# Performance work log

Hardware: AMD Instinct MI355X
Metric: run time of the kernel (lower is better)

Reference implementation:

```python
import jax, jax.numpy as jnp
import numpy as np

B, S = 8, 128
D_SENS, D_ACT, D_STR, D_ENC, DIM = 512, 32, 128, 128, 128
D_JOINT = D_STR + D_ENC  # 256


def _l2norm(x):
    return x / jnp.clip(jnp.linalg.norm(x, axis=-1, keepdims=True), 1e-12)


def _mlp(x, layers):
    # layers: list of (W, b); ReLU between layers, none on output
    n = len(layers)
    for i, (W, b) in enumerate(layers):
        x = x @ W + b
        if i < n - 1:
            x = jax.nn.relu(x)
    return x


def _meta_mlp(x, p):
    x = jax.nn.relu(x @ p['W1'] + p['b1'])
    x = jax.nn.relu(x @ p['W2'] + p['b2'])
    return x @ p['W3'] + p['b3']


def setup_inputs() -> dict:
    key = jax.random.key(0)
    it = iter(jax.random.split(key, 40))
    w = lambda shape, s=0.02: jax.random.normal(next(it), shape, jnp.float32) * s
    H = D_ACT * 4  # to_transitions hidden dim (default mlp_hidden_dim)
    return dict(
        sensory=jax.random.normal(next(it), (B, S, D_SENS), jnp.float32),
        actions=jax.random.normal(next(it), (B, S, D_ACT), jnp.float32),
        init_hidden=w((1, D_STR), 0.01),
        tW1=w((D_ACT, H)), tb1=w((H,)),
        tW2=w((H, H)), tb2=w((H,)),
        tW3=w((H, D_STR * D_STR)), tb3=w((D_STR * D_STR,)),
        enc_w=w((D_SENS, D_ENC)), enc_b=w((D_ENC,)),
        dec_w=w((D_ENC, D_SENS)), dec_b=w((D_SENS,)),
        q_w=w((D_JOINT, DIM)), k_w=w((D_JOINT, DIM)), v_w=w((D_JOINT, DIM)),
        mW1=w((DIM, 2 * DIM)), mb1=w((2 * DIM,)),
        mW2=w((2 * DIM, 2 * DIM)), mb2=w((2 * DIM,)),
        mW3=w((2 * DIM, DIM)), mb3=w((DIM,)),
        oW1=w((DIM, 2 * DIM)), ob1=w((2 * DIM,)),
        oW2=w((2 * DIM, 2 * DIM)), ob2=w((2 * DIM,)),
        oW3=w((2 * DIM, D_JOINT)), ob3=w((D_JOINT,)),
        sW1=w((2 * D_STR + 1, 2 * D_STR)), sb1=w((2 * D_STR,)),
        sW2=w((2 * D_STR, 2 * D_STR)), sb2=w((2 * D_STR,)),
        sW3=w((2 * D_STR, D_STR)), sb3=w((D_STR,)),
        integration_ratio=jnp.asarray(0.1, jnp.float32),
    )


def reference(sensory, actions, init_hidden, tW1, tb1, tW2, tb2, tW3, tb3,
              enc_w, enc_b, dec_w, dec_b, q_w, k_w, v_w,
              mW1, mb1, mW2, mb2, mW3, mb3,
              oW1, ob1, oW2, ob2, oW3, ob3,
              sW1, sb1, sW2, sb2, sW3, sb3, integration_ratio):
    mse = lambda a, b: jnp.mean((a - b) ** 2)

    # --- PathIntegration: actions -> transitions -> scripted RNN scan ---
    trans = _mlp(actions, [(tW1, tb1), (tW2, tb2), (tW3, tb3)])  # (B,S,ds*ds)
    trans = trans.reshape(B, S, D_STR, D_STR)
    h0 = jnp.broadcast_to(_l2norm(init_hidden), (B, D_STR))

    def step(h, T):  # h (B,ds), T (B,ds,ds)
        h = _l2norm(jax.nn.relu(jnp.einsum('bi,bij->bj', h, T)))
        return h, h

    _, hs = jax.lax.scan(step, h0, jnp.swapaxes(trans, 0, 1))
    structural = jnp.swapaxes(hs, 0, 1)  # (B,S,ds)

    # --- sensory encoder (Linear) ---
    encoded = sensory @ enc_w + enc_b  # (B,S,D_ENC)

    meta_params = {'W1': mW1, 'b1': mb1, 'W2': mW2, 'b2': mb2, 'W3': mW3, 'b3': mb3}

    def retrieve(s, e):
        joint = jnp.concatenate((s, e), axis=-1)
        q = joint @ q_w
        r = _meta_mlp(q, meta_params)
        out = _mlp(r, [(oW1, ob1), (oW2, ob2), (oW3, ob3)])
        return out[..., :D_STR], out[..., D_STR:]

    # generative branch
    dec_gen_s, dec_enc = retrieve(structural, jnp.zeros_like(encoded))
    generative_pred_loss = mse(sensory, dec_enc @ dec_w + dec_b)

    # relational branch (source calls retrieve(zeros, encoded) twice)
    dec_s1, _ = retrieve(jnp.zeros_like(structural), encoded)
    dec_s2, _ = retrieve(jnp.zeros_like(structural), encoded)
    relational_loss = mse(dec_s1, structural) + mse(dec_s2, structural)

    # consistency / inference correction
    corr_s, corr_e = retrieve(dec_gen_s, encoded)
    sse = jnp.sum((corr_e - encoded) ** 2, axis=-1, keepdims=True)  # (B,S,1)
    pred_var = _mlp(jnp.concatenate((corr_s, dec_gen_s, sse), axis=-1),
                    [(sW1, sb1), (sW2, sb2), (sW3, sb3)])
    inf_s = dec_gen_s + (corr_s - dec_gen_s) * integration_ratio * pred_var
    consistency_loss = mse(dec_gen_s, inf_s)

    final_s, inf_e = retrieve(inf_s, jnp.zeros_like(encoded))
    inference_pred_loss = mse(sensory, inf_e @ dec_w + dec_b)

    # per-sample fast-weight memory gradients (nested vmap(grad))
    store = jnp.concatenate((final_s, encoded), axis=-1)
    keys = store @ k_w
    values = store @ v_w

    def meta_loss(p, k, v):
        return jnp.mean((_meta_mlp(k, p) - v) ** 2)

    per_grad = jax.vmap(jax.vmap(jax.grad(meta_loss), in_axes=(None, 0, 0)),
                        in_axes=(None, 0, 0))
    g = per_grad(meta_params, keys, values)  # each leaf (B,S,*param_shape)

    total = (generative_pred_loss + relational_loss
             + consistency_loss + inference_pred_loss)  # all loss weights 1.0
    return (total, g['W1'], g['b1'], g['W2'], g['b2'], g['W3'], g['b3'])
```

## Files before the change

### kernel.cpp

```cpp
#include <hip/hip_runtime.h>
#include <hip/hip_bf16.h>

constexpr size_t OFF_W1 = 1;
constexpr size_t OFF_B1 = OFF_W1 + (size_t)1024*32768;
constexpr size_t OFF_W2 = OFF_B1 + (size_t)1024*256;
constexpr size_t OFF_B2 = OFF_W2 + (size_t)1024*65536;
constexpr size_t OFF_W3 = OFF_B2 + (size_t)1024*256;
constexpr size_t OFF_B3 = OFF_W3 + (size_t)1024*32768;

__global__ __launch_bounds__(256) void gemm_kernel(
    const float* __restrict__ A, int lda,
    const float* __restrict__ W, int ldw,
    const float* __restrict__ bias,
    float* __restrict__ C, int ldc,
    int N, int K, int do_relu)
{
    __shared__ float As[16][65];
    __shared__ float Ws[16][65];
    const int tid = threadIdx.x;
    const int tx = tid & 15, ty = tid >> 4;
    const int m0 = blockIdx.x * 64, n0 = blockIdx.y * 64;
    float acc[4][4] = {};
    for (int k0 = 0; k0 < K; k0 += 16) {
        for (int l = tid; l < 1024; l += 256) {
            int mm = l >> 4, kk = l & 15;
            int gk = k0 + kk;
            As[kk][mm] = (gk < K) ? A[(size_t)(m0+mm)*lda + gk] : 0.f;
        }
        for (int l = tid; l < 1024; l += 256) {
            int kk = l >> 6, nn = l & 63;
            int gk = k0 + kk, gn = n0 + nn;
            Ws[kk][nn] = (gk < K && gn < N) ? W[(size_t)gk*ldw + gn] : 0.f;
        }
        __syncthreads();
        #pragma unroll
        for (int kk = 0; kk < 16; ++kk) {
            float a[4], b[4];
            #pragma unroll
            for (int i=0;i<4;i++) a[i] = As[kk][ty*4+i];
            #pragma unroll
            for (int j=0;j<4;j++) b[j] = Ws[kk][tx*4+j];
            #pragma unroll
            for (int i=0;i<4;i++)
                #pragma unroll
                for (int j=0;j<4;j++)
                    acc[i][j] = fmaf(a[i], b[j], acc[i][j]);
        }
        __syncthreads();
    }
    #pragma unroll
    for (int i=0;i<4;i++){
        int gm = m0 + ty*4 + i;
        #pragma unroll
        for (int j=0;j<4;j++){
            int gn = n0 + tx*4 + j;
            if (gn < N) {
                float v = acc[i][j] + (bias ? bias[gn] : 0.f);
                if (do_relu) v = fmaxf(v, 0.f);
                C[(size_t)gm*ldc + gn] = v;
            }
        }
    }
}

__global__ __launch_bounds__(512) void scan_kernel2(
    const float* __restrict__ trans,
    const float* __restrict__ init_hidden,
    float* __restrict__ structural)
{
    __shared__ float h[128];
    __shared__ float psum[16*128];
    const int b = blockIdx.x, tid = threadIdx.x;
    const int q = tid >> 5, g = tid & 31;
    const int jj = g * 4, i0 = q * 8;

    if (tid < 32) {
        float4 v = *(const float4*)&init_hidden[tid*4];
        float ss = v.x*v.x + v.y*v.y + v.z*v.z + v.w*v.w;
        ss += __shfl_xor(ss, 16); ss += __shfl_xor(ss, 8); ss += __shfl_xor(ss, 4);
        ss += __shfl_xor(ss, 2);  ss += __shfl_xor(ss, 1);
        float inv = 1.f / fmaxf(sqrtf(ss), 1e-12f);
        v.x *= inv; v.y *= inv; v.z *= inv; v.w *= inv;
        *(float4*)&h[tid*4] = v;
    }
    __syncthreads();

    float4 cur[8], nxt[8];
    {
        const float* T0 = trans + ((size_t)(b*128) << 14);
        #pragma unroll
        for (int i = 0; i < 8; ++i)
            cur[i] = *(const float4*)&T0[(size_t)(i0+i)*128 + jj];
    }

    for (int t = 0; t < 128; ++t) {
        const int tn = (t < 127) ? t + 1 : 127;
        const float* Tn = trans + ((size_t)(b*128 + tn) << 14);
        #pragma unroll
        for (int i = 0; i < 8; ++i)
            nxt[i] = *(const float4*)&Tn[(size_t)(i0+i)*128 + jj];

        float4 acc = make_float4(0.f,0.f,0.f,0.f);
        #pragma unroll
        for (int i = 0; i < 8; ++i) {
            float hv = h[i0+i];
            acc.x = fmaf(hv, cur[i].x, acc.x);
            acc.y = fmaf(hv, cur[i].y, acc.y);
            acc.z = fmaf(hv, cur[i].z, acc.z);
            acc.w = fmaf(hv, cur[i].w, acc.w);
        }
        *(float4*)&psum[q*128 + jj] = acc;
        __syncthreads();
        if (tid < 32) {
            float4 s = make_float4(0.f,0.f,0.f,0.f);
            #pragma unroll
            for (int qq = 0; qq < 16; ++qq) {
                float4 p = *(const float4*)&psum[qq*128 + tid*4];
                s.x += p.x; s.y += p.y; s.z += p.z; s.w += p.w;
            }
            s.x = fmaxf(s.x, 0.f); s.y = fmaxf(s.y, 0.f);
            s.z = fmaxf(s.z, 0.f); s.w = fmaxf(s.w, 0.f);
            float ss = s.x*s.x + s.y*s.y + s.z*s.z + s.w*s.w;
            ss += __shfl_xor(ss, 16); ss += __shfl_xor(ss, 8); ss += __shfl_xor(ss, 4);
            ss += __shfl_xor(ss, 2);  ss += __shfl_xor(ss, 1);
            float inv = 1.f / fmaxf(sqrtf(ss), 1e-12f);
            s.x *= inv; s.y *= inv; s.z *= inv; s.w *= inv;
            *(float4*)&h[tid*4] = s;
            *(float4*)&structural[((size_t)(b*128 + t))*128 + tid*4] = s;
        }
        __syncthreads();
        #pragma unroll
        for (int i = 0; i < 8; ++i) cur[i] = nxt[i];
    }
}

__device__ __forceinline__ void stage_rows(float* buf, const float* src, int ld,
                                           int row0, int rows, int t)
{
    int r = t >> 5; if (rows == 4) r &= 3;
    const int k4 = (t & 31) * 4;
    float4 v = make_float4(0.f,0.f,0.f,0.f);
    if (src) v = *(const float4*)&src[(size_t)(row0 + r)*ld + k4];
    *(float4*)&buf[r*128 + k4] = v;
}

__device__ __forceinline__ void layer_n256_r8(
    const float* __restrict__ W, const float* __restrict__ bias, int K,
    const float* __restrict__ x, int xs, float* __restrict__ y, int relu, int t)
{
    const int c4 = (t & 63) * 4;
    const int r0 = (t >> 6) * 2;
    float4 a0 = bias ? *(const float4*)&bias[c4] : make_float4(0.f,0.f,0.f,0.f);
    float4 a1 = a0;
    const float* x0 = x + r0 * xs;
    const float* x1 = x0 + xs;
    for (int k = 0; k < K; ++k) {
        float4 w = *(const float4*)&W[(size_t)k*256 + c4];
        float xa = x0[k], xb = x1[k];
        a0.x = fmaf(w.x, xa, a0.x); a0.y = fmaf(w.y, xa, a0.y);
        a0.z = fmaf(w.z, xa, a0.z); a0.w = fmaf(w.w, xa, a0.w);
        a1.x = fmaf(w.x, xb, a1.x); a1.y = fmaf(w.y, xb, a1.y);
        a1.z = fmaf(w.z, xb, a1.z); a1.w = fmaf(w.w, xb, a1.w);
    }
    if (relu) {
        a0.x=fmaxf(a0.x,0.f); a0.y=fmaxf(a0.y,0.f); a0.z=fmaxf(a0.z,0.f); a0.w=fmaxf(a0.w,0.f);
        a1.x=fmaxf(a1.x,0.f); a1.y=fmaxf(a1.y,0.f); a1.z=fmaxf(a1.z,0.f); a1.w=fmaxf(a1.w,0.f);
    }
    *(float4*)&y[r0*256 + c4] = a0;
    *(float4*)&y[(r0+1)*256 + c4] = a1;
}

__device__ __forceinline__ void layer_n256_r4(
    const float* __restrict__ W, const float* __restrict__ bias, int K,
    const float* __restrict__ x, int xs, float* __restrict__ y, int relu,
    const float* __restrict__ mask, int t)
{
    const int c4 = (t & 63) * 4;
    const int r = t >> 6;
    float4 a = bias ? *(const float4*)&bias[c4] : make_float4(0.f,0.f,0.f,0.f);
    const float* xr = x + r * xs;
    for (int k = 0; k < K; ++k) {
        float4 w = *(const float4*)&W[(size_t)k*256 + c4];
        float xa = xr[k];
        a.x = fmaf(w.x, xa, a.x); a.y = fmaf(w.y, xa, a.y);
        a.z = fmaf(w.z, xa, a.z); a.w = fmaf(w.w, xa, a.w);
    }
    if (relu) {
        a.x=fmaxf(a.x,0.f); a.y=fmaxf(a.y,0.f); a.z=fmaxf(a.z,0.f); a.w=fmaxf(a.w,0.f);
    }
    if (mask) {
        float4 m = *(const float4*)&mask[r*256 + c4];
        a.x = (m.x > 0.f) ? a.x : 0.f; a.y = (m.y > 0.f) ? a.y : 0.f;
        a.z = (m.z > 0.f) ? a.z : 0.f; a.w = (m.w > 0.f) ? a.w : 0.f;
    }
    *(float4*)&y[r*256 + c4] = a;
}

__device__ __forceinline__ void layer_n128(
    const float* __restrict__ W, const float* __restrict__ bias, int K,
    const float* __restrict__ x, int xs, float* __restrict__ y, int ys, int relu,
    int rows, int t)
{
    const int c4 = (t & 31) * 4;
    int r = t >> 5; if (rows == 4) r &= 3;
    float4 a = bias ? *(const float4*)&bias[c4] : make_float4(0.f,0.f,0.f,0.f);
    const float* xr = x + r * xs;
    for (int k = 0; k < K; ++k) {
        float4 w = *(const float4*)&W[(size_t)k*128 + c4];
        float xa = xr[k];
        a.x = fmaf(w.x, xa, a.x); a.y = fmaf(w.y, xa, a.y);
        a.z = fmaf(w.z, xa, a.z); a.w = fmaf(w.w, xa, a.w);
    }
    if (relu) {
        a.x=fmaxf(a.x,0.f); a.y=fmaxf(a.y,0.f); a.z=fmaxf(a.z,0.f); a.w=fmaxf(a.w,0.f);
    }
    *(float4*)&y[r*ys + c4] = a;
}

__device__ __forceinline__ void layer_n128_dual(
    const float* __restrict__ W,
    const float* __restrict__ xA, const float* __restrict__ xB,
    float* __restrict__ y, int rows, int t)
{
    const int c4 = (t & 31) * 4;
    int r = t >> 5; if (rows == 4) r &= 3;
    float4 a = make_float4(0.f,0.f,0.f,0.f);
    const float* xa_ = xA + r * 128;
    const float* xb_ = xB + r * 128;
    for (int k = 0; k < 128; ++k) {
        float4 w = *(const float4*)&W[(size_t)k*128 + c4];
        float v = xa_[k];
        a.x = fmaf(w.x, v, a.x); a.y = fmaf(w.y, v, a.y);
        a.z = fmaf(w.z, v, a.z); a.w = fmaf(w.w, v, a.w);
    }
    for (int k = 0; k < 128; ++k) {
        float4 w = *(const float4*)&W[(size_t)(128+k)*128 + c4];
        float v = xb_[k];
        a.x = fmaf(w.x, v, a.x); a.y = fmaf(w.y, v, a.y);
        a.z = fmaf(w.z, v, a.z); a.w = fmaf(w.w, v, a.w);
    }
    *(float4*)&y[r*128 + c4] = a;
}

__global__ __launch_bounds__(256) void fused_retrieve_kernel(
    const float* __restrict__ A1, int ld1,
    const float* __restrict__ A2, int ld2,
    const float* __restrict__ qw,
    const float* __restrict__ mW1, const float* __restrict__ mb1,
    const float* __restrict__ mW2, const float* __restrict__ mb2,
    const float* __restrict__ mW3, const float* __restrict__ mb3,
    const float* __restrict__ oW1, const float* __restrict__ ob1,
    const float* __restrict__ oW2, const float* __restrict__ ob2,
    const float* __restrict__ oW3, const float* __restrict__ ob3,
    float* __restrict__ outB)
{
    __shared__ float bufA[8*128], bufB[8*128], ping[8*256], pong[8*256];
    const int t = threadIdx.x;
    const int row0 = blockIdx.x * 8;

    stage_rows(bufA, A1, ld1, row0, 8, t);
    stage_rows(bufB, A2, ld2, row0, 8, t);
    __syncthreads();
    layer_n128_dual(qw, bufA, bufB, ping, 8, t);
    __syncthreads();
    layer_n256_r8(mW1, mb1, 128, ping, 128, pong, 1, t);
    __syncthreads();
    layer_n256_r8(mW2, mb2, 256, pong, 256, ping, 1, t);
    __syncthreads();
    layer_n128(mW3, mb3, 256, ping, 256, pong, 128, 0, 8, t);
    __syncthreads();
    layer_n256_r8(oW1, ob1, 128, pong, 128, ping, 1, t);
    __syncthreads();
    layer_n256_r8(oW2, ob2, 256, ping, 256, pong, 1, t);
    __syncthreads();
    layer_n256_r8(oW3, ob3, 256, pong, 256, ping, 0, t);
    __syncthreads();
    #pragma unroll
    for (int e = t; e < 512; e += 256) {
        int r = e >> 6, c = (e & 63) * 4;
        *(float4*)&outB[(size_t)(row0+r)*256 + c] = *(const float4*)&ping[r*256 + c];
    }
}

__global__ __launch_bounds__(256) void fused_svar_kernel(
    const float* __restrict__ out3,
    const float* __restrict__ out1,
    const float* __restrict__ encoded,
    const float* __restrict__ sW1, const float* __restrict__ sb1,
    const float* __restrict__ sW2, const float* __restrict__ sb2,
    const float* __restrict__ sW3, const float* __restrict__ sb3,
    float* __restrict__ pvar)
{
    __shared__ float bufA[8*128], bufB[8*128], sse[8], ping[8*256], pong[8*256];
    const int t = threadIdx.x;
    const int row0 = blockIdx.x * 8;
    const int r = t >> 5, k4 = (t & 31) * 4;

    {
        float4 cs = *(const float4*)&out3[(size_t)(row0+r)*256 + k4];
        float4 ds = *(const float4*)&out1[(size_t)(row0+r)*256 + k4];
        *(float4*)&bufA[r*128 + k4] = cs;
        *(float4*)&bufB[r*128 + k4] = ds;
        float4 ce = *(const float4*)&out3[(size_t)(row0+r)*256 + 128 + k4];
        float4 en = *(const float4*)&encoded[(size_t)(row0+r)*128 + k4];
        float dx = ce.x-en.x, dy = ce.y-en.y, dz = ce.z-en.z, dw = ce.w-en.w;
        float ss = dx*dx + dy*dy + dz*dz + dw*dw;
        ss += __shfl_xor(ss, 16); ss += __shfl_xor(ss, 8); ss += __shfl_xor(ss, 4);
        ss += __shfl_xor(ss, 2);  ss += __shfl_xor(ss, 1);
        if ((t & 31) == 0) sse[r] = ss;
    }
    __syncthreads();
    {
        const int c4 = (t & 63) * 4;
        const int r0 = (t >> 6) * 2;
        float4 a0 = *(const float4*)&sb1[c4];
        float4 a1 = a0;
        for (int k = 0; k < 128; ++k) {
            float4 w = *(const float4*)&sW1[(size_t)k*256 + c4];
            float xa = bufA[r0*128 + k], xb = bufA[(r0+1)*128 + k];
            a0.x=fmaf(w.x,xa,a0.x); a0.y=fmaf(w.y,xa,a0.y); a0.z=fmaf(w.z,xa,a0.z); a0.w=fmaf(w.w,xa,a0.w);
            a1.x=fmaf(w.x,xb,a1.x); a1.y=fmaf(w.y,xb,a1.y); a1.z=fmaf(w.z,xb,a1.z); a1.w=fmaf(w.w,xb,a1.w);
        }
        for (int k = 0; k < 128; ++k) {
            float4 w = *(const float4*)&sW1[(size_t)(128+k)*256 + c4];
            float xa = bufB[r0*128 + k], xb = bufB[(r0+1)*128 + k];
            a0.x=fmaf(w.x,xa,a0.x); a0.y=fmaf(w.y,xa,a0.y); a0.z=fmaf(w.z,xa,a0.z); a0.w=fmaf(w.w,xa,a0.w);
            a1.x=fmaf(w.x,xb,a1.x); a1.y=fmaf(w.y,xb,a1.y); a1.z=fmaf(w.z,xb,a1.z); a1.w=fmaf(w.w,xb,a1.w);
        }
        {
            float4 w = *(const float4*)&sW1[(size_t)256*256 + c4];
            float xa = sse[r0], xb = sse[r0+1];
            a0.x=fmaf(w.x,xa,a0.x); a0.y=fmaf(w.y,xa,a0.y); a0.z=fmaf(w.z,xa,a0.z); a0.w=fmaf(w.w,xa,a0.w);
            a1.x=fmaf(w.x,xb,a1.x); a1.y=fmaf(w.y,xb,a1.y); a1.z=fmaf(w.z,xb,a1.z); a1.w=fmaf(w.w,xb,a1.w);
        }
        a0.x=fmaxf(a0.x,0.f); a0.y=fmaxf(a0.y,0.f); a0.z=fmaxf(a0.z,0.f); a0.w=fmaxf(a0.w,0.f);
        a1.x=fmaxf(a1.x,0.f); a1.y=fmaxf(a1.y,0.f); a1.z=fmaxf(a1.z,0.f); a1.w=fmaxf(a1.w,0.f);
        *(float4*)&ping[r0*256 + c4] = a0;
        *(float4*)&ping[(r0+1)*256 + c4] = a1;
    }
    __syncthreads();
    layer_n256_r8(sW2, sb2, 256, ping, 256, pong, 1, t);
    __syncthreads();
    layer_n128(sW3, sb3, 256, pong, 256, ping, 128, 0, 8, t);
    __syncthreads();
    {
        int rr = t >> 5, c = (t & 31) * 4;
        *(float4*)&pvar[(size_t)(row0+rr)*128 + c] = *(const float4*)&ping[rr*128 + c];
    }
}

__global__ __launch_bounds__(256) void fused_grad_kernel(
    const float* __restrict__ A1,
    const float* __restrict__ encoded,
    const float* __restrict__ k_w, const float* __restrict__ v_w,
    const float* __restrict__ mW1, const float* __restrict__ mb1,
    const float* __restrict__ mW2, const float* __restrict__ mb2,
    const float* __restrict__ mW3, const float* __restrict__ mb3,
    const float* __restrict__ T2,
    const float* __restrict__ T3,
    float* __restrict__ out)
{
    __shared__ float bufA[4*128], bufB[4*128], ks[4*128], vs[4*128];
    __shared__ float h1[4*256], h2[4*256], dob[4*128], dh2[4*256], dh1[4*256];
    const int t = threadIdx.x;
    const int row0 = blockIdx.x * 4;

    stage_rows(bufA, A1, 256, row0, 4, t);
    stage_rows(bufB, encoded, 128, row0, 4, t);
    __syncthreads();
    layer_n128_dual(k_w, bufA, bufB, ks, 4, t);
    layer_n128_dual(v_w, bufA, bufB, vs, 4, t);
    __syncthreads();
    layer_n256_r4(mW1, mb1, 128, ks, 128, h1, 1, nullptr, t);
    __syncthreads();
    layer_n256_r4(mW2, mb2, 256, h1, 256, h2, 1, nullptr, t);
    __syncthreads();
    layer_n128(mW3, mb3, 256, h2, 256, dob, 128, 0, 4, t);
    __syncthreads();
    for (int e = t; e < 512; e += 256)
        dob[e] = (dob[e] - vs[e]) * 0.015625f;
    __syncthreads();
    layer_n256_r4(T3, nullptr, 128, dob, 128, dh2, 0, h2, t);
    __syncthreads();
    layer_n256_r4(T2, nullptr, 256, dh2, 256, dh1, 0, h1, t);
    __syncthreads();

    #pragma unroll
    for (int r = 0; r < 4; ++r) {
        const size_t row = row0 + r;
        {
            const float dv = dh1[r*256 + t];
            float* p = out + OFF_W1 + row*32768;
            for (int i = 0; i < 128; ++i)
                p[(size_t)i*256 + t] = ks[r*128 + i] * dv;
            out[OFF_B1 + row*256 + t] = dv;
        }
        {
            const float d2 = dh2[r*256 + t];
            float* p = out + OFF_W2 + row*65536;
            for (int i = 0; i < 256; ++i)
                p[(size_t)i*256 + t] = h1[r*256 + i] * d2;
            out[OFF_B2 + row*256 + t] = d2;
        }
        {
            const int j = t & 127, ih = t >> 7;
            const float d3 = dob[r*128 + j];
            float* p = out + OFF_W3 + row*32768;
            for (int i = ih*128; i < ih*128 + 128; ++i)
                p[(size_t)i*128 + j] = h2[r*256 + i] * d3;
            if (t < 128) out[OFF_B3 + row*128 + t] = dob[r*128 + t];
        }
    }
}

__global__ __launch_bounds__(256) void mse_kernel(
    const float* __restrict__ A, int lda,
    const float* __restrict__ Bm, int ldb,
    int N, float scale, float* __restrict__ accum)
{
    const int m = blockIdx.x;
    float s = 0.f;
    for (int jj = threadIdx.x; jj < N; jj += 256) {
        float d = A[(size_t)m*lda + jj] - Bm[(size_t)m*ldb + jj];
        s = fmaf(d, d, s);
    }
    #pragma unroll
    for (int off = 32; off > 0; off >>= 1) s += __shfl_down(s, off, 64);
    __shared__ float w[4];
    if ((threadIdx.x & 63) == 0) w[threadIdx.x >> 6] = s;
    __syncthreads();
    if (threadIdx.x == 0) atomicAdd(accum, (w[0]+w[1]+w[2]+w[3]) * scale);
}

__global__ __launch_bounds__(128) void infs_kernel(
    const float* __restrict__ out1,
    const float* __restrict__ out3,
    const float* __restrict__ pvar,
    const float* __restrict__ ratio_p,
    float* __restrict__ inf_s,
    float scale, float* __restrict__ accum)
{
    const int m = blockIdx.x, t = threadIdx.x;
    float ratio = ratio_p[0];
    float dgs = out1[(size_t)m*256 + t];
    float cs  = out3[(size_t)m*256 + t];
    float pv  = pvar[(size_t)m*128 + t];
    float delta = (cs - dgs) * ratio * pv;
    inf_s[(size_t)m*128 + t] = dgs + delta;
    float ss = delta * delta;
    #pragma unroll
    for (int off = 32; off > 0; off >>= 1) ss += __shfl_down(ss, off, 64);
    __shared__ float w2[2];
    if ((t & 63) == 0) w2[t >> 6] = ss;
    __syncthreads();
    if (t == 0) atomicAdd(accum, (w2[0] + w2[1]) * scale);
}

__global__ void transpose_kernel(const float* __restrict__ src, float* __restrict__ dst, int R, int C)
{
    const int c = blockIdx.x, r = threadIdx.x;
    dst[(size_t)c*R + r] = src[(size_t)r*C + c];
}

__global__ void zero_kernel(float* acc) {
    if (threadIdx.x < 8) acc[threadIdx.x] = 0.f;
}

__global__ void total_kernel(const float* acc, float* out) {
    if (threadIdx.x == 0)
        out[0] = acc[0] + acc[1] + acc[2] + acc[3];
}

static inline void gemmF(const float* A, int lda, const float* W, int ldw, const float* bias,
                         float* C, int N, int K, int relu, hipStream_t s)
{
    dim3 g(16, (N + 63) / 64);
    gemm_kernel<<<g, 256, 0, s>>>(A, lda, W, ldw, bias, C, N, N, K, relu);
}

extern "C" void kernel_launch(void* const* d_in, const int* in_sizes, int n_in,
                              void* d_out, int out_size, void* d_ws, size_t ws_size,
                              hipStream_t stream)
{
    const float* sensory     = (const float*)d_in[0];
    const float* actions     = (const float*)d_in[1];
    const float* init_hidden = (const float*)d_in[2];
    const float* tW1 = (const float*)d_in[3];  const float* tb1 = (const float*)d_in[4];
    const float* tW2 = (const float*)d_in[5];  const float* tb2 = (const float*)d_in[6];
    const float* tW3 = (const float*)d_in[7];  const float* tb3 = (const float*)d_in[8];
    const float* enc_w = (const float*)d_in[9];  const float* enc_b = (const float*)d_in[10];
    const float* dec_w = (const float*)d_in[11]; const float* dec_b = (const float*)d_in[12];
    const float* q_w = (const float*)d_in[13];
    const float* k_w = (const float*)d_in[14];
    const float* v_w = (const float*)d_in[15];
    const float* mW1 = (const float*)d_in[16]; const float* mb1 = (const float*)d_in[17];
    const float* mW2 = (const float*)d_in[18]; const float* mb2 = (const float*)d_in[19];
    const float* mW3 = (const float*)d_in[20]; const float* mb3 = (const float*)d_in[21];
    const float* oW1 = (const float*)d_in[22]; const float* ob1 = (const float*)d_in[23];
    const float* oW2 = (const float*)d_in[24]; const float* ob2 = (const float*)d_in[25];
    const float* oW3 = (const float*)d_in[26]; const float* ob3 = (const float*)d_in[27];
    const float* sW1 = (const float*)d_in[28]; const float* sb1 = (const float*)d_in[29];
    const float* sW2 = (const float*)d_in[30]; const float* sb2 = (const float*)d_in[31];
    const float* sW3 = (const float*)d_in[32]; const float* sb3 = (const float*)d_in[33];
    const float* ratio = (const float*)d_in[34];
    float* out = (float*)d_out;

    float* Wsp = (float*)d_ws;
    size_t off = 0;
    float* acc  = Wsp + off; off += 16;
    float* a1   = Wsp + off; off += (size_t)1024*128;
    float* a2   = Wsp + off; off += (size_t)1024*128;
    float* trans= Wsp + off; off += (size_t)1024*16384;
    float* structural = Wsp + off; off += (size_t)1024*128;
    float* encoded    = Wsp + off; off += (size_t)1024*128;
    float* out1 = Wsp + off; off += (size_t)1024*256;
    float* out2 = Wsp + off; off += (size_t)1024*256;
    float* out3 = Wsp + off; off += (size_t)1024*256;
    float* out4 = Wsp + off; off += (size_t)1024*256;
    float* pvar = Wsp + off; off += (size_t)1024*128;
    float* infs = Wsp + off; off += (size_t)1024*128;
    float* deco = Wsp + off; off += (size_t)1024*512;
    float* T2   = Wsp + off; off += (size_t)256*256;
    float* T3   = Wsp + off; off += (size_t)128*256;

    zero_kernel<<<1, 64, 0, stream>>>(acc);
    transpose_kernel<<<256, 256, 0, stream>>>(mW2, T2, 256, 256);
    transpose_kernel<<<128, 256, 0, stream>>>(mW3, T3, 256, 128);

    gemmF(actions, 32, tW1, 128, tb1, a1, 128, 32, 1, stream);
    gemmF(a1, 128, tW2, 128, tb2, a2, 128, 128, 1, stream);
    gemmF(a2, 128, tW3, 16384, tb3, trans, 16384, 128, 0, stream);
    gemmF(sensory, 512, enc_w, 128, enc_b, encoded, 128, 512, 0, stream);
    scan_kernel2<<<8, 512, 0, stream>>>(trans, init_hidden, structural);

    fused_retrieve_kernel<<<128, 256, 0, stream>>>(structural, 128, nullptr, 0, q_w,
        mW1, mb1, mW2, mb2, mW3, mb3, oW1, ob1, oW2, ob2, oW3, ob3, out1);
    gemmF(out1 + 128, 256, dec_w, 512, dec_b, deco, 512, 128, 0, stream);
    mse_kernel<<<1024, 256, 0, stream>>>(deco, 512, sensory, 512, 512, 1.f/524288.f, acc + 0);

    fused_retrieve_kernel<<<128, 256, 0, stream>>>(nullptr, 0, encoded, 128, q_w,
        mW1, mb1, mW2, mb2, mW3, mb3, oW1, ob1, oW2, ob2, oW3, ob3, out2);
    mse_kernel<<<1024, 256, 0, stream>>>(out2, 256, structural, 128, 128, 2.f/131072.f, acc + 1);

    fused_retrieve_kernel<<<128, 256, 0, stream>>>(out1, 256, encoded, 128, q_w,
        mW1, mb1, mW2, mb2, mW3, mb3, oW1, ob1, oW2, ob2, oW3, ob3, out3);
    fused_svar_kernel<<<128, 256, 0, stream>>>(out3, out1, encoded,
        sW1, sb1, sW2, sb2, sW3, sb3, pvar);
    infs_kernel<<<1024, 128, 0, stream>>>(out1, out3, pvar, ratio, infs, 1.f/131072.f, acc + 2);

    fused_retrieve_kernel<<<128, 256, 0, stream>>>(infs, 128, nullptr, 0, q_w,
        mW1, mb1, mW2, mb2, mW3, mb3, oW1, ob1, oW2, ob2, oW3, ob3, out4);
    gemmF(out4 + 128, 256, dec_w, 512, dec_b, deco, 512, 128, 0, stream);
    mse_kernel<<<1024, 256, 0, stream>>>(deco, 512, sensory, 512, 512, 1.f/524288.f, acc + 3);

    fused_grad_kernel<<<256, 256, 0, stream>>>(out4, encoded, k_w, v_w,
        mW1, mb1, mW2, mb2, mW3, mb3, T2, T3, out);

    total_kernel<<<1, 64, 0, stream>>>(acc, out);
}
```

Measured before the change: 1.533 ms.

## Transpose transition weights, fuse decoder GEMM with MSE, batch retrieve passes, vectorize grad stores

```diff
diff --git a/kernel.cpp b/kernel.cpp
--- a/kernel.cpp
+++ b/kernel.cpp
@@ -63,16 +63,135 @@
     }
 }
 
-__global__ __launch_bounds__(512) void scan_kernel2(
-    const float* __restrict__ trans,
+__global__ __launch_bounds__(256) void prep_kernel(
+    const float* __restrict__ tW3,
+    const float* __restrict__ mW2, const float* __restrict__ mW3,
+    float* __restrict__ tW3T,
+    float* __restrict__ T2, float* __restrict__ T3,
+    float* __restrict__ acc)
+{
+    __shared__ float tile[64*129];
+    const int t = threadIdx.x;
+    const int bid = blockIdx.x;
+    if (bid < 256) {
+        const int k = bid >> 1, i0 = (bid & 1) * 64;
+        const size_t base = (size_t)k << 14;
+        for (int l = t; l < 8192; l += 256) {
+            int ii = l >> 7, jj = l & 127;
+            tile[ii*129 + jj] = tW3[base + (size_t)(i0+ii)*128 + jj];
+        }
+        __syncthreads();
+        for (int l = t; l < 8192; l += 256) {
+            int jj = l >> 6, ii = l & 63;
+            tW3T[base + (size_t)jj*128 + i0 + ii] = tile[ii*129 + jj];
+        }
+    } else if (bid < 512) {
+        const int c = bid - 256;
+        T2[(size_t)c*256 + t] = mW2[(size_t)t*256 + c];
+    } else if (bid < 640) {
+        const int c = bid - 512;
+        T3[(size_t)c*256 + t] = mW3[(size_t)t*128 + c];
+    } else {
+        if (t < 16) acc[t] = 0.f;
+    }
+}
+
+__device__ __forceinline__ void gemm_k128_compute(
+    const float* __restrict__ A, int lda, const float* __restrict__ W,
+    const float* __restrict__ bias, int bias_mode, int N, int m0, int n0, int t,
+    float* __restrict__ As, float4* __restrict__ acc)
+{
+    for (int l = t; l < 4096; l += 256) {
+        int r = l >> 7, k = l & 127;
+        As[k*36 + r] = A[(size_t)(m0 + r)*lda + k];
+    }
+    __syncthreads();
+    const int c4 = (t & 63) * 4;
+    const int r0 = (t >> 6) * 8;
+    float4 bv;
+    if (bias_mode == 0) {
+        bv = *(const float4*)&bias[n0 + c4];
+    } else {
+        const int n = n0 + c4;
+        const int j = n >> 7, i = n & 127;
+        bv.x = bias[(size_t)(i+0)*128 + j];
+        bv.y = bias[(size_t)(i+1)*128 + j];
+        bv.z = bias[(size_t)(i+2)*128 + j];
+        bv.w = bias[(size_t)(i+3)*128 + j];
+    }
+    #pragma unroll
+    for (int i = 0; i < 8; ++i) acc[i] = bv;
+    const float* Wp = W + (size_t)n0 + c4;
+    #pragma unroll 4
+    for (int k = 0; k < 128; ++k) {
+        float4 w = *(const float4*)&Wp[(size_t)k*N];
+        float a[8];
+        *(float4*)&a[0] = *(const float4*)&As[k*36 + r0];
+        *(float4*)&a[4] = *(const float4*)&As[k*36 + r0 + 4];
+        #pragma unroll
+        for (int i = 0; i < 8; ++i) {
+            acc[i].x = fmaf(w.x, a[i], acc[i].x);
+            acc[i].y = fmaf(w.y, a[i], acc[i].y);
+            acc[i].z = fmaf(w.z, a[i], acc[i].z);
+            acc[i].w = fmaf(w.w, a[i], acc[i].w);
+        }
+    }
+}
+
+__global__ __launch_bounds__(256) void gemm_k128_kernel(
+    const float* __restrict__ A, int lda, const float* __restrict__ W,
+    const float* __restrict__ bias, int bias_mode, float* __restrict__ C, int N)
+{
+    __shared__ float As[128*36];
+    float4 acc[8];
+    const int t = threadIdx.x;
+    const int m0 = blockIdx.x * 32, n0 = blockIdx.y * 256;
+    gemm_k128_compute(A, lda, W, bias, bias_mode, N, m0, n0, t, As, acc);
+    const int c4 = (t & 63) * 4;
+    const int r0 = (t >> 6) * 8;
+    #pragma unroll
+    for (int i = 0; i < 8; ++i)
+        *(float4*)&C[(size_t)(m0 + r0 + i)*N + n0 + c4] = acc[i];
+}
+
+__global__ __launch_bounds__(256) void gemm_k128_mse_kernel(
+    const float* __restrict__ A, int lda, const float* __restrict__ W,
+    const float* __restrict__ bias, const float* __restrict__ ref, int N,
+    float scale, float* __restrict__ accum)
+{
+    __shared__ float As[128*36];
+    float4 acc[8];
+    const int t = threadIdx.x;
+    const int m0 = blockIdx.x * 32, n0 = blockIdx.y * 256;
+    gemm_k128_compute(A, lda, W, bias, 0, N, m0, n0, t, As, acc);
+    const int c4 = (t & 63) * 4;
+    const int r0 = (t >> 6) * 8;
+    float s = 0.f;
+    #pragma unroll
+    for (int i = 0; i < 8; ++i) {
+        float4 rv = *(const float4*)&ref[(size_t)(m0 + r0 + i)*N + n0 + c4];
+        float dx = acc[i].x - rv.x, dy = acc[i].y - rv.y;
+        float dz = acc[i].z - rv.z, dw = acc[i].w - rv.w;
+        s += dx*dx + dy*dy + dz*dz + dw*dw;
+    }
+    #pragma unroll
+    for (int off = 32; off > 0; off >>= 1) s += __shfl_down(s, off, 64);
+    __shared__ float wred[4];
+    if ((t & 63) == 0) wred[t >> 6] = s;
+    __syncthreads();
+    if (t == 0) atomicAdd(accum, (wred[0]+wred[1]+wred[2]+wred[3]) * scale);
+}
+
+__global__ __launch_bounds__(512) void scan_kernel3(
+    const float* __restrict__ transT,
     const float* __restrict__ init_hidden,
     float* __restrict__ structural)
 {
     __shared__ float h[128];
-    __shared__ float psum[16*128];
+    __shared__ float ws[8];
     const int b = blockIdx.x, tid = threadIdx.x;
-    const int q = tid >> 5, g = tid & 31;
-    const int jj = g * 4, i0 = q * 8;
+    const int j = tid >> 2, p = tid & 3;
+    const int i0 = p * 32;
 
     if (tid < 32) {
         float4 v = *(const float4*)&init_hidden[tid*4];
@@ -85,52 +204,47 @@
     }
     __syncthreads();
 
+    const size_t bbase = ((size_t)b) << 21;
+    const int lane_off = j*128 + i0;
     float4 cur[8], nxt[8];
     {
-        const float* T0 = trans + ((size_t)(b*128) << 14);
+        const float* T0 = transT + bbase + lane_off;
         #pragma unroll
-        for (int i = 0; i < 8; ++i)
-            cur[i] = *(const float4*)&T0[(size_t)(i0+i)*128 + jj];
-    }
-
+        for (int r = 0; r < 8; ++r) cur[r] = *(const float4*)&T0[r*4];
+    }
     for (int t = 0; t < 128; ++t) {
         const int tn = (t < 127) ? t + 1 : 127;
-        const float* Tn = trans + ((size_t)(b*128 + tn) << 14);
+        const float* Tn = transT + bbase + ((size_t)tn << 14) + lane_off;
         #pragma unroll
-        for (int i = 0; i < 8; ++i)
-            nxt[i] = *(const float4*)&Tn[(size_t)(i0+i)*128 + jj];
-
-        float4 acc = make_float4(0.f,0.f,0.f,0.f);
+        for (int r = 0; r < 8; ++r) nxt[r] = *(const float4*)&Tn[r*4];
+
+        float4 a = make_float4(0.f, 0.f, 0.f, 0.f);
         #pragma unroll
-        for (int i = 0; i < 8; ++i) {
-            float hv = h[i0+i];
-            acc.x = fmaf(hv, cur[i].x, acc.x);
-            acc.y = fmaf(hv, cur[i].y, acc.y);
-            acc.z = fmaf(hv, cur[i].z, acc.z);
-            acc.w = fmaf(hv, cur[i].w, acc.w);
-        }
-        *(float4*)&psum[q*128 + jj] = acc;
+        for (int r = 0; r < 8; ++r) {
+            float4 hv = *(const float4*)&h[i0 + r*4];
+            a.x = fmaf(hv.x, cur[r].x, a.x);
+            a.y = fmaf(hv.y, cur[r].y, a.y);
+            a.z = fmaf(hv.z, cur[r].z, a.z);
+            a.w = fmaf(hv.w, cur[r].w, a.w);
+        }
+        float s = (a.x + a.y) + (a.z + a.w);
+        s += __shfl_xor(s, 1);
+        s += __shfl_xor(s, 2);
+        float v = fmaxf(s, 0.f);
+        float q = v * v;
+        q += __shfl_xor(q, 4);  q += __shfl_xor(q, 8);
+        q += __shfl_xor(q, 16); q += __shfl_xor(q, 32);
+        if ((tid & 63) == 0) ws[tid >> 6] = q;
         __syncthreads();
-        if (tid < 32) {
-            float4 s = make_float4(0.f,0.f,0.f,0.f);
-            #pragma unroll
-            for (int qq = 0; qq < 16; ++qq) {
-                float4 p = *(const float4*)&psum[qq*128 + tid*4];
-                s.x += p.x; s.y += p.y; s.z += p.z; s.w += p.w;
-            }
-            s.x = fmaxf(s.x, 0.f); s.y = fmaxf(s.y, 0.f);
-            s.z = fmaxf(s.z, 0.f); s.w = fmaxf(s.w, 0.f);
-            float ss = s.x*s.x + s.y*s.y + s.z*s.z + s.w*s.w;
-            ss += __shfl_xor(ss, 16); ss += __shfl_xor(ss, 8); ss += __shfl_xor(ss, 4);
-            ss += __shfl_xor(ss, 2);  ss += __shfl_xor(ss, 1);
-            float inv = 1.f / fmaxf(sqrtf(ss), 1e-12f);
-            s.x *= inv; s.y *= inv; s.z *= inv; s.w *= inv;
-            *(float4*)&h[tid*4] = s;
-            *(float4*)&structural[((size_t)(b*128 + t))*128 + tid*4] = s;
-        }
+        float ss = ((ws[0]+ws[1]) + (ws[2]+ws[3])) + ((ws[4]+ws[5]) + (ws[6]+ws[7]));
+        float inv = 1.f / fmaxf(sqrtf(ss), 1e-12f);
+        float hv = v * inv;
+        __syncthreads();
+        if (p == 0) h[j] = hv;
+        else if (p == 1) structural[(((size_t)(b*128 + t)) << 7) + j] = hv;
         __syncthreads();
         #pragma unroll
-        for (int i = 0; i < 8; ++i) cur[i] = nxt[i];
+        for (int r = 0; r < 8; ++r) cur[r] = nxt[r];
     }
 }
 
@@ -242,7 +356,52 @@
     *(float4*)&y[r*128 + c4] = a;
 }
 
-__global__ __launch_bounds__(256) void fused_retrieve_kernel(
+__global__ __launch_bounds__(256) void fused_retrieve2_kernel(
+    const float* __restrict__ A1a, int ld1a, const float* __restrict__ A2a, int ld2a,
+    float* __restrict__ outa,
+    const float* __restrict__ A1b, int ld1b, const float* __restrict__ A2b, int ld2b,
+    float* __restrict__ outb,
+    const float* __restrict__ qw,
+    const float* __restrict__ mW1, const float* __restrict__ mb1,
+    const float* __restrict__ mW2, const float* __restrict__ mb2,
+    const float* __restrict__ mW3, const float* __restrict__ mb3,
+    const float* __restrict__ oW1, const float* __restrict__ ob1,
+    const float* __restrict__ oW2, const float* __restrict__ ob2,
+    const float* __restrict__ oW3, const float* __restrict__ ob3)
+{
+    __shared__ float bufA[8*128], bufB[8*128], ping[8*256], pong[8*256];
+    const int t = threadIdx.x;
+    const bool second = blockIdx.x >= 128;
+    const int row0 = (blockIdx.x & 127) * 8;
+    const float* A1 = second ? A1b : A1a;  const int ld1 = second ? ld1b : ld1a;
+    const float* A2 = second ? A2b : A2a;  const int ld2 = second ? ld2b : ld2a;
+    float* outB = second ? outb : outa;
+
+    stage_rows(bufA, A1, ld1, row0, 8, t);
+    stage_rows(bufB, A2, ld2, row0, 8, t);
+    __syncthreads();
+    layer_n128_dual(qw, bufA, bufB, ping, 8, t);
+    __syncthreads();
+    layer_n256_r8(mW1, mb1, 128, ping, 128, pong, 1, t);
+    __syncthreads();
+    layer_n256_r8(mW2, mb2, 256, pong, 256, ping, 1, t);
+    __syncthreads();
+    layer_n128(mW3, mb3, 256, ping, 256, pong, 128, 0, 8, t);
+    __syncthreads();
+    layer_n256_r8(oW1, ob1, 128, pong, 128, ping, 1, t);
+    __syncthreads();
+    layer_n256_r8(oW2, ob2, 256, ping, 256, pong, 1, t);
+    __syncthreads();
+    layer_n256_r8(oW3, ob3, 256, pong, 256, ping, 0, t);
+    __syncthreads();
+    #pragma unroll
+    for (int e = t; e < 512; e += 256) {
+        int r = e >> 6, c = (e & 63) * 4;
+        *(float4*)&outB[(size_t)(row0+r)*256 + c] = *(const float4*)&ping[r*256 + c];
+    }
+}
+
+__global__ __launch_bounds__(256) void fused_retrieve4_kernel(
     const float* __restrict__ A1, int ld1,
     const float* __restrict__ A2, int ld2,
     const float* __restrict__ qw,
@@ -254,30 +413,29 @@
     const float* __restrict__ oW3, const float* __restrict__ ob3,
     float* __restrict__ outB)
 {
-    __shared__ float bufA[8*128], bufB[8*128], ping[8*256], pong[8*256];
+    __shared__ float bufA[4*128], bufB[4*128], ping[4*256], pong[4*256];
     const int t = threadIdx.x;
-    const int row0 = blockIdx.x * 8;
-
-    stage_rows(bufA, A1, ld1, row0, 8, t);
-    stage_rows(bufB, A2, ld2, row0, 8, t);
-    __syncthreads();
-    layer_n128_dual(qw, bufA, bufB, ping, 8, t);
-    __syncthreads();
-    layer_n256_r8(mW1, mb1, 128, ping, 128, pong, 1, t);
-    __syncthreads();
-    layer_n256_r8(mW2, mb2, 256, pong, 256, ping, 1, t);
-    __syncthreads();
-    layer_n128(mW3, mb3, 256, ping, 256, pong, 128, 0, 8, t);
-    __syncthreads();
-    layer_n256_r8(oW1, ob1, 128, pong, 128, ping, 1, t);
-    __syncthreads();
-    layer_n256_r8(oW2, ob2, 256, ping, 256, pong, 1, t);
-    __syncthreads();
-    layer_n256_r8(oW3, ob3, 256, pong, 256, ping, 0, t);
-    __syncthreads();
-    #pragma unroll
-    for (int e = t; e < 512; e += 256) {
-        int r = e >> 6, c = (e & 63) * 4;
+    const int row0 = blockIdx.x * 4;
+
+    stage_rows(bufA, A1, ld1, row0, 4, t);
+    stage_rows(bufB, A2, ld2, row0, 4, t);
+    __syncthreads();
+    layer_n128_dual(qw, bufA, bufB, ping, 4, t);
+    __syncthreads();
+    layer_n256_r4(mW1, mb1, 128, ping, 128, pong, 1, nullptr, t);
+    __syncthreads();
+    layer_n256_r4(mW2, mb2, 256, pong, 256, ping, 1, nullptr, t);
+    __syncthreads();
+    layer_n128(mW3, mb3, 256, ping, 256, pong, 128, 0, 4, t);
+    __syncthreads();
+    layer_n256_r4(oW1, ob1, 128, pong, 128, ping, 1, nullptr, t);
+    __syncthreads();
+    layer_n256_r4(oW2, ob2, 256, ping, 256, pong, 1, nullptr, t);
+    __syncthreads();
+    layer_n256_r4(oW3, ob3, 256, pong, 256, ping, 0, nullptr, t);
+    __syncthreads();
+    {
+        int r = t >> 6, c = (t & 63) * 4;
         *(float4*)&outB[(size_t)(row0+r)*256 + c] = *(const float4*)&ping[r*256 + c];
     }
 }
@@ -389,25 +547,39 @@
     for (int r = 0; r < 4; ++r) {
         const size_t row = row0 + r;
         {
-            const float dv = dh1[r*256 + t];
+            const int c4 = (t & 63) * 4;
+            const int i0 = (t >> 6) * 32;
+            const float4 dv = *(const float4*)&dh1[r*256 + c4];
             float* p = out + OFF_W1 + row*32768;
-            for (int i = 0; i < 128; ++i)
-                p[(size_t)i*256 + t] = ks[r*128 + i] * dv;
-            out[OFF_B1 + row*256 + t] = dv;
+            for (int i = i0; i < i0 + 32; ++i) {
+                float kv = ks[r*128 + i];
+                float4 o; o.x = kv*dv.x; o.y = kv*dv.y; o.z = kv*dv.z; o.w = kv*dv.w;
+                *(float4*)&p[(size_t)i*256 + c4] = o;
+            }
+            out[OFF_B1 + row*256 + t] = dh1[r*256 + t];
         }
         {
-            const float d2 = dh2[r*256 + t];
+            const int c4 = (t & 63) * 4;
+            const int i0 = (t >> 6) * 64;
+            const float4 dv = *(const float4*)&dh2[r*256 + c4];
             float* p = out + OFF_W2 + row*65536;
-            for (int i = 0; i < 256; ++i)
-                p[(size_t)i*256 + t] = h1[r*256 + i] * d2;
-            out[OFF_B2 + row*256 + t] = d2;
+            for (int i = i0; i < i0 + 64; ++i) {
+                float hv = h1[r*256 + i];
+                float4 o; o.x = hv*dv.x; o.y = hv*dv.y; o.z = hv*dv.z; o.w = hv*dv.w;
+                *(float4*)&p[(size_t)i*256 + c4] = o;
+            }
+            out[OFF_B2 + row*256 + t] = dh2[r*256 + t];
         }
         {
-            const int j = t & 127, ih = t >> 7;
-            const float d3 = dob[r*128 + j];
+            const int c4 = (t & 31) * 4;
+            const int i0 = (t >> 5) * 32;
+            const float4 dv = *(const float4*)&dob[r*128 + c4];
             float* p = out + OFF_W3 + row*32768;
-            for (int i = ih*128; i < ih*128 + 128; ++i)
-                p[(size_t)i*128 + j] = h2[r*256 + i] * d3;
+            for (int i = i0; i < i0 + 32; ++i) {
+                float hv = h2[r*256 + i];
+                float4 o; o.x = hv*dv.x; o.y = hv*dv.y; o.z = hv*dv.z; o.w = hv*dv.w;
+                *(float4*)&p[(size_t)i*128 + c4] = o;
+            }
             if (t < 128) out[OFF_B3 + row*128 + t] = dob[r*128 + t];
         }
     }
@@ -454,16 +626,6 @@
     if ((t & 63) == 0) w2[t >> 6] = ss;
     __syncthreads();
     if (t == 0) atomicAdd(accum, (w2[0] + w2[1]) * scale);
-}
-
-__global__ void transpose_kernel(const float* __restrict__ src, float* __restrict__ dst, int R, int C)
-{
-    const int c = blockIdx.x, r = threadIdx.x;
-    dst[(size_t)c*R + r] = src[(size_t)r*C + c];
-}
-
-__global__ void zero_kernel(float* acc) {
-    if (threadIdx.x < 8) acc[threadIdx.x] = 0.f;
 }
 
 __global__ void total_kernel(const float* acc, float* out) {
@@ -506,52 +668,54 @@
     float* out = (float*)d_out;
 
     float* Wsp = (float*)d_ws;
-    size_t off = 0;
-    float* acc  = Wsp + off; off += 16;
-    float* a1   = Wsp + off; off += (size_t)1024*128;
-    float* a2   = Wsp + off; off += (size_t)1024*128;
-    float* trans= Wsp + off; off += (size_t)1024*16384;
-    float* structural = Wsp + off; off += (size_t)1024*128;
-    float* encoded    = Wsp + off; off += (size_t)1024*128;
-    float* out1 = Wsp + off; off += (size_t)1024*256;
-    float* out2 = Wsp + off; off += (size_t)1024*256;
-    float* out3 = Wsp + off; off += (size_t)1024*256;
-    float* out4 = Wsp + off; off += (size_t)1024*256;
-    float* pvar = Wsp + off; off += (size_t)1024*128;
-    float* infs = Wsp + off; off += (size_t)1024*128;
-    float* deco = Wsp + off; off += (size_t)1024*512;
-    float* T2   = Wsp + off; off += (size_t)256*256;
-    float* T3   = Wsp + off; off += (size_t)128*256;
-
-    zero_kernel<<<1, 64, 0, stream>>>(acc);
-    transpose_kernel<<<256, 256, 0, stream>>>(mW2, T2, 256, 256);
-    transpose_kernel<<<128, 256, 0, stream>>>(mW3, T3, 256, 128);
-
-    gemmF(actions, 32, tW1, 128, tb1, a1, 128, 32, 1, stream);
-    gemmF(a1, 128, tW2, 128, tb2, a2, 128, 128, 1, stream);
-    gemmF(a2, 128, tW3, 16384, tb3, trans, 16384, 128, 0, stream);
+    float* acc   = Wsp;
+    float* ALIAS = Wsp + 16;
+    float* a1_buf     = ALIAS;
+    float* structural = ALIAS + 131072;
+    float* out1 = ALIAS + 262144;
+    float* out2 = ALIAS + 524288;
+    float* out3 = ALIAS + 786432;
+    float* out4 = ALIAS + 1048576;
+    float* pvar = ALIAS + 1310720;
+    float* infs = ALIAS + 1441792;
+    float* tW3T = ALIAS;
+    size_t off = 16 + 2097152;
+    float* a2      = Wsp + off; off += 131072;
+    float* encoded = Wsp + off; off += 131072;
+    float* transT  = Wsp + off; off += 16777216;
+    float* T2      = Wsp + off; off += 65536;
+    float* T3      = Wsp + off; off += 32768;
+
+    gemmF(actions, 32, tW1, 128, tb1, a1_buf, 128, 32, 1, stream);
+    gemmF(a1_buf, 128, tW2, 128, tb2, a2, 128, 128, 1, stream);
+
+    prep_kernel<<<641, 256, 0, stream>>>(tW3, mW2, mW3, tW3T, T2, T3, acc);
+
     gemmF(sensory, 512, enc_w, 128, enc_b, encoded, 128, 512, 0, stream);
-    scan_kernel2<<<8, 512, 0, stream>>>(trans, init_hidden, structural);
-
-    fused_retrieve_kernel<<<128, 256, 0, stream>>>(structural, 128, nullptr, 0, q_w,
-        mW1, mb1, mW2, mb2, mW3, mb3, oW1, ob1, oW2, ob2, oW3, ob3, out1);
-    gemmF(out1 + 128, 256, dec_w, 512, dec_b, deco, 512, 128, 0, stream);
-    mse_kernel<<<1024, 256, 0, stream>>>(deco, 512, sensory, 512, 512, 1.f/524288.f, acc + 0);
-
-    fused_retrieve_kernel<<<128, 256, 0, stream>>>(nullptr, 0, encoded, 128, q_w,
-        mW1, mb1, mW2, mb2, mW3, mb3, oW1, ob1, oW2, ob2, oW3, ob3, out2);
+
+    gemm_k128_kernel<<<dim3(32, 64), 256, 0, stream>>>(a2, 128, tW3T, tb3, 1, transT, 16384);
+
+    scan_kernel3<<<8, 512, 0, stream>>>(transT, init_hidden, structural);
+
+    fused_retrieve2_kernel<<<256, 256, 0, stream>>>(
+        structural, 128, nullptr, 0, out1,
+        nullptr, 0, encoded, 128, out2,
+        q_w, mW1, mb1, mW2, mb2, mW3, mb3, oW1, ob1, oW2, ob2, oW3, ob3);
+
     mse_kernel<<<1024, 256, 0, stream>>>(out2, 256, structural, 128, 128, 2.f/131072.f, acc + 1);
-
-    fused_retrieve_kernel<<<128, 256, 0, stream>>>(out1, 256, encoded, 128, q_w,
-        mW1, mb1, mW2, mb2, mW3, mb3, oW1, ob1, oW2, ob2, oW3, ob3, out3);
+    gemm_k128_mse_kernel<<<dim3(32, 2), 256, 0, stream>>>(
+        out1 + 128, 256, dec_w, dec_b, sensory, 512, 1.f/524288.f, acc + 0);
+
+    fused_retrieve4_kernel<<<256, 256, 0, stream>>>(out1, 256, encoded, 128,
+        q_w, mW1, mb1, mW2, mb2, mW3, mb3, oW1, ob1, oW2, ob2, oW3, ob3, out3);
     fused_svar_kernel<<<128, 256, 0, stream>>>(out3, out1, encoded,
         sW1, sb1, sW2, sb2, sW3, sb3, pvar);
     infs_kernel<<<1024, 128, 0, stream>>>(out1, out3, pvar, ratio, infs, 1.f/131072.f, acc + 2);
 
-    fused_retrieve_kernel<<<128, 256, 0, stream>>>(infs, 128, nullptr, 0, q_w,
-        mW1, mb1, mW2, mb2, mW3, mb3, oW1, ob1, oW2, ob2, oW3, ob3, out4);
-    gemmF(out4 + 128, 256, dec_w, 512, dec_b, deco, 512, 128, 0, stream);
-    mse_kernel<<<1024, 256, 0, stream>>>(deco, 512, sensory, 512, 512, 1.f/524288.f, acc + 3);
+    fused_retrieve4_kernel<<<256, 256, 0, stream>>>(infs, 128, nullptr, 0,
+        q_w, mW1, mb1, mW2, mb2, mW3, mb3, oW1, ob1, oW2, ob2, oW3, ob3, out4);
+    gemm_k128_mse_kernel<<<dim3(32, 2), 256, 0, stream>>>(
+        out4 + 128, 256, dec_w, dec_b, sensory, 512, 1.f/524288.f, acc + 3);
 
     fused_grad_kernel<<<256, 256, 0, stream>>>(out4, encoded, k_w, v_w,
         mW1, mb1, mW2, mb2, mW3, mb3, T2, T3, out);
```

Measured after the change: 1.465 ms. -4.5%, faster.
